# Optimization experiments

Hardware: AMD Instinct MI355X
Metric: run time of the kernel (lower is better)

The kernel has to match this reference:

```python
import jax, jax.numpy as jnp
import numpy as np

B, R, C, NH = 8, 64, 256, 8
N = R * R            # 4096 tokens
HD = C // NH         # head dim 32
FF = 3               # focusing factor

def dwconv(x, w, b):
    # x: (B, C, H, W); w: (C, 1, kh, kw) depthwise
    y = jax.lax.conv_general_dilated(
        x, w, window_strides=(1, 1), padding='SAME',
        dimension_numbers=('NCHW', 'OIHW', 'NCHW'),
        feature_group_count=x.shape[1])
    return y + b[None, :, None, None]

def setup_inputs() -> dict:
    key = jax.random.key(0)
    ks = jax.random.split(key, 6)
    return {
        'qkv': jax.random.normal(ks[0], (3, B, N, C), jnp.float32),
        'pos_enc': jax.random.normal(ks[1], (1, N, C), jnp.float32) * 0.02,
        'scale': jax.random.normal(ks[2], (1, 1, C), jnp.float32) * 0.02,
        'w_v': jax.random.normal(ks[3], (C, 1, 3, 3), jnp.float32) * 0.1,
        'b_v': jnp.zeros((C,), jnp.float32),
        'w_dwc': jax.random.normal(ks[4], (HD, 1, 5, 5), jnp.float32) * 0.1,
        'b_dwc': jnp.zeros((HD,), jnp.float32),
    }

def reference(qkv, pos_enc, scale, w_v, b_v, w_dwc, b_dwc):
    q, k, v = qkv[0], qkv[1], qkv[2]          # each (B, N, C)
    # --- LePE: depthwise 3x3 conv on v over full channel dim ---
    v_img = v.transpose(0, 2, 1).reshape(B, C, R, R)
    lepe = dwconv(v_img, w_v, b_v)            # (B, C, R, R)
    lepe = lepe.reshape(B * NH, HD, N).transpose(0, 2, 1)   # (B*h, N, hd)
    v = v_img.reshape(B, C, N).transpose(0, 2, 1)           # (B, N, C)
    # --- focused kernelization ---
    k = k + pos_enc
    sc = jax.nn.softplus(scale)
    q = (jax.nn.relu(q) + 1e-6) / sc
    k = (jax.nn.relu(k) + 1e-6) / sc
    qn = jnp.linalg.norm(q, axis=-1, keepdims=True)
    kn = jnp.linalg.norm(k, axis=-1, keepdims=True)
    q = q ** FF
    k = k ** FF
    q = q / jnp.linalg.norm(q, axis=-1, keepdims=True) * qn
    k = k / jnp.linalg.norm(k, axis=-1, keepdims=True) * kn
    split = lambda x: x.reshape(B, N, NH, HD).transpose(0, 2, 1, 3).reshape(B * NH, N, HD)
    q, k, v = split(q), split(k), split(v)    # (B*h, N, hd)
    # --- linear attention (kv aggregation path: N >> hd) ---
    z = 1.0 / (jnp.einsum('bic,bc->bi', q, k.sum(axis=1)) + 1e-6)
    kv = jnp.einsum('bjc,bjd->bcd', k, v)     # (B*h, hd, hd)
    x = jnp.einsum('bic,bcd,bi->bid', q, kv, z)
    # --- dwc feature mixing on v per head ---
    fm = v.transpose(0, 2, 1).reshape(B * NH, HD, R, R)
    fm = dwconv(fm, w_dwc, b_dwc).reshape(B * NH, HD, N).transpose(0, 2, 1)
    x = x + fm + lepe
    x = x.reshape(B, NH, N, HD).transpose(0, 2, 1, 3).reshape(B, N, C)
    return x
```

## Files before the change

### kernel.cpp

```cpp
#include <hip/hip_runtime.h>
#include <math.h>

#define B_  8
#define R_  64
#define C_  256
#define NH_ 8
#define N_  4096
#define HD_ 32
#define LDP 260

__device__ __forceinline__ float softplus_rcp(float s) {
    return 1.f / __logf(1.f + __expf(s));
}

__global__ __launch_bounds__(256) void kernelNB3(
        const float* __restrict__ qkv, const float* __restrict__ pos,
        const float* __restrict__ scale,
        float* __restrict__ qs_arr, float* __restrict__ part,
        float* __restrict__ kspart) {
    __shared__ float smem[8576];
    float* kf_s  = smem;
    float* v_s   = smem + 4160;
    float* rsc_s = smem + 8320;

    const int t    = threadIdx.x;
    const int wave = t >> 6, lane = t & 63;
    const int tk   = lane >> 4;
    const int lr   = lane & 15;
    const int blk  = blockIdx.x;
    const int tok0 = blk * 32;

    rsc_s[t] = softplus_rcp(scale[t]);

    const size_t qbase = (size_t)tok0 * C_;
    const size_t koff  = (size_t)B_ * N_ * C_;
    const size_t voff  = (size_t)2 * B_ * N_ * C_;

    const int h  = t >> 5;
    const int l  = t & 31;
    const int cg = l & 7;
    const int dg = l >> 3;

    float acc[4][8];
    #pragma unroll
    for (int ii = 0; ii < 4; ii++)
        #pragma unroll
        for (int jj = 0; jj < 8; jj++) acc[ii][jj] = 0.f;
    float ksp[4] = {0.f, 0.f, 0.f, 0.f};

    __syncthreads();
    float rs[16];
    #pragma unroll
    for (int j = 0; j < 4; j++)
        *(float4*)&rs[j * 4] = *(const float4*)&rsc_s[j * 64 + lr * 4];

    #pragma unroll
    for (int tile = 0; tile < 2; tile++) {
        const int row  = wave * 4 + tk;
        const int nrow = tile * 16 + row;
        const int tok  = tok0 + nrow;
        const size_t off  = qbase + (size_t)nrow * C_;
        const size_t poff = (size_t)(tok & (N_ - 1)) * C_;

        float kc[16];
        float sq2 = 0.f, sq6 = 0.f, sk2 = 0.f, sk6 = 0.f;
        #pragma unroll
        for (int j = 0; j < 4; j++) {
            const int c = j * 64 + lr * 4;
            const float4 q4 = *(const float4*)(qkv + off + c);
            const float4 k4 = *(const float4*)(qkv + koff + off + c);
            const float4 v4 = *(const float4*)(qkv + voff + off + c);
            const float4 p4 = *(const float4*)(pos + poff + c);
            *(float4*)&v_s[row * LDP + c] = v4;
            const float qa[4] = {q4.x, q4.y, q4.z, q4.w};
            const float ka[4] = {k4.x, k4.y, k4.z, k4.w};
            const float pa[4] = {p4.x, p4.y, p4.z, p4.w};
            #pragma unroll
            for (int e = 0; e < 4; e++) {
                const float r  = rs[j * 4 + e];
                const float qv = (fmaxf(qa[e], 0.f) + 1e-6f) * r;
                const float kw = (fmaxf(ka[e] + pa[e], 0.f) + 1e-6f) * r;
                sq2 += qv * qv;  sk2 += kw * kw;
                const float q3 = qv * qv * qv, k3 = kw * kw * kw;
                sq6 += q3 * q3;  sk6 += k3 * k3;
                kc[j * 4 + e] = k3;
            }
        }
        #pragma unroll
        for (int m = 1; m < 16; m <<= 1) {
            sq2 += __shfl_xor(sq2, m, 64);
            sq6 += __shfl_xor(sq6, m, 64);
            sk2 += __shfl_xor(sk2, m, 64);
            sk6 += __shfl_xor(sk6, m, 64);
        }
        if (lr == 0) qs_arr[tok] = sqrtf(sq2) * rsqrtf(sq6);
        const float ks = sqrtf(sk2) * rsqrtf(sk6);
        #pragma unroll
        for (int j = 0; j < 4; j++) {
            const float4 kf4 = make_float4(kc[j*4+0] * ks, kc[j*4+1] * ks,
                                           kc[j*4+2] * ks, kc[j*4+3] * ks);
            *(float4*)&kf_s[row * LDP + j * 64 + lr * 4] = kf4;
        }
        __syncthreads();
        {
            const float* kfp = kf_s + h * HD_ + cg * 4;
            const float* vp  = v_s  + h * HD_ + dg * 8;
            #pragma unroll 4
            for (int nl = 0; nl < 16; nl++) {
                const float4 kr = *(const float4*)(kfp + nl * LDP);
                const float4 va = *(const float4*)(vp  + nl * LDP);
                const float4 vb = *(const float4*)(vp  + nl * LDP + 4);
                ksp[0] += kr.x;  ksp[1] += kr.y;
                ksp[2] += kr.z;  ksp[3] += kr.w;
                const float kk[4] = {kr.x, kr.y, kr.z, kr.w};
                const float vv[8] = {va.x, va.y, va.z, va.w,
                                     vb.x, vb.y, vb.z, vb.w};
                #pragma unroll
                for (int ii = 0; ii < 4; ii++)
                    #pragma unroll
                    for (int jj = 0; jj < 8; jj++)
                        acc[ii][jj] = fmaf(kk[ii], vv[jj], acc[ii][jj]);
            }
        }
        __syncthreads();
    }

    #pragma unroll
    for (int ii = 0; ii < 4; ii++) {
        const float4 a = make_float4(acc[ii][0], acc[ii][1], acc[ii][2], acc[ii][3]);
        const float4 b = make_float4(acc[ii][4], acc[ii][5], acc[ii][6], acc[ii][7]);
        const int base = h * 1024 + (cg * 4 + ii) * 32 + dg * 8;
        *(float4*)&smem[base]     = a;
        *(float4*)&smem[base + 4] = b;
    }
    if (dg == 0)
        *(float4*)&kspart[(size_t)blk * 256 + h * 32 + cg * 4] =
            make_float4(ksp[0], ksp[1], ksp[2], ksp[3]);
    __syncthreads();
    float* pdst = part + (size_t)blk * 8192;
    #pragma unroll
    for (int i = 0; i < 8; i++)
        *(float4*)&pdst[i * 1024 + t * 4] = *(const float4*)&smem[i * 1024 + t * 4];
}

__global__ __launch_bounds__(256) void kernelR(
        const float* __restrict__ part, const float* __restrict__ kspart,
        float* __restrict__ kv_ws, float* __restrict__ ksum_ws) {
    const int t  = threadIdx.x;
    const int bh = blockIdx.x >> 2, q = blockIdx.x & 3;
    const int b  = bh >> 3, h = bh & 7;

    const float* p = part + (size_t)(b * 128) * 8192 + h * 1024 + q * 256 + t;
    float s = 0.f;
    #pragma unroll 4
    for (int j = 0; j < 128; j++) s += p[(size_t)j * 8192];
    kv_ws[bh * 1024 + q * 256 + t] = s;

    if (q == 0 && t < 32) {
        const float* kp = kspart + (size_t)(b * 128) * 256 + h * 32 + t;
        float s2 = 0.f;
        #pragma unroll 8
        for (int j = 0; j < 128; j++) s2 += kp[(size_t)j * 256];
        ksum_ws[bh * 32 + t] = s2;
    }
}

__global__ __launch_bounds__(256) void kernelCD2(
        const float* __restrict__ qkv, const float* __restrict__ qs_arr,
        const float* __restrict__ kv_ws, const float* __restrict__ ksum_ws,
        const float* __restrict__ scale,
        const float* __restrict__ w_v,  const float* __restrict__ b_v,
        const float* __restrict__ w_dwc, const float* __restrict__ b_dwc,
        float* __restrict__ out) {
    __shared__ float v_s[20 * 20 * 32];
    __shared__ float kv_s[1024];
    __shared__ float ks_s[32];
    __shared__ float rsc_s[32];
    const int t    = threadIdx.x;
    const int tile = blockIdx.x;
    const int h    = blockIdx.y;
    const int b    = blockIdx.z;
    const int ty0  = (tile >> 2) * 16, tx0 = (tile & 3) * 16;
    const int bh   = b * NH_ + h;

    ((float4*)kv_s)[t] = ((const float4*)(kv_ws + (size_t)bh * 1024))[t];
    if (t < 32) {
        ks_s[t]  = ksum_ws[bh * HD_ + t];
        rsc_s[t] = softplus_rcp(scale[h * HD_ + t]);
    }

    const float* vb = qkv + (size_t)2 * B_ * N_ * C_ + (size_t)b * N_ * C_ + h * HD_;
    #pragma unroll
    for (int i = 0; i < 13; i++) {
        const int idx = i * 256 + t;
        if (idx < 3200) {
            const int pix = idx >> 3, d4 = (idx & 7) * 4;
            const int yy = pix / 20, xx = pix - yy * 20;
            const int gy = ty0 + yy - 2, gx = tx0 + xx - 2;
            float4 val = make_float4(0.f, 0.f, 0.f, 0.f);
            if (gy >= 0 && gy < R_ && gx >= 0 && gx < R_)
                val = *(const float4*)(vb + (size_t)(gy * R_ + gx) * C_ + d4);
            *(float4*)&v_s[pix * 32 + d4] = val;
        }
    }

    const int c  = t & 31, pg = t >> 5;
    float wv[9], wd[25];
    {
        const float* wvp = w_v + (size_t)(h * HD_ + c) * 9;
        const float* wdp = w_dwc + (size_t)c * 25;
        #pragma unroll
        for (int i = 0; i < 9; i++)  wv[i] = wvp[i];
        #pragma unroll
        for (int i = 0; i < 25; i++) wd[i] = wdp[i];
    }
    const float bias = b_v[h * HD_ + c] + b_dwc[c];
    __syncthreads();

    float res[32];
    #pragma unroll
    for (int r2 = 0; r2 < 2; r2++) {
        const int ty = pg * 2 + r2;
        float win[5][5];
        #pragma unroll
        for (int j = 0; j < 5; j++)
            #pragma unroll
            for (int i = 0; i < 5; i++)
                win[j][i] = v_s[((ty + i) * 20 + j) * 32 + c];
        #pragma unroll
        for (int tx = 0; tx < 16; tx++) {
            float a = bias;
            #pragma unroll
            for (int j = 0; j < 5; j++) {
                const int slot = (tx + j) % 5;
                #pragma unroll
                for (int i = 0; i < 5; i++)
                    a = fmaf(wd[i * 5 + j], win[slot][i], a);
            }
            #pragma unroll
            for (int j = 1; j < 4; j++) {
                const int slot = (tx + j) % 5;
                #pragma unroll
                for (int i = 1; i < 4; i++)
                    a = fmaf(wv[(i - 1) * 3 + (j - 1)], win[slot][i], a);
            }
            res[r2 * 16 + tx] = a;
            if (tx < 15) {
                const int slot = tx % 5;
                #pragma unroll
                for (int i = 0; i < 5; i++)
                    win[slot][i] = v_s[((ty + i) * 20 + (tx + 5)) * 32 + c];
            }
        }
    }
    __syncthreads();
    #pragma unroll
    for (int r2 = 0; r2 < 2; r2++)
        #pragma unroll
        for (int tx = 0; tx < 16; tx++)
            v_s[((pg * 2 + r2) * 16 + tx) * 33 + c] = res[r2 * 16 + tx];
    __syncthreads();

    {
        const int tyy = t >> 4, txx = t & 15;
        const int n   = (ty0 + tyy) * R_ + (tx0 + txx);
        const int tok = b * N_ + n;
        float q[32];
        const float4* qsrc = (const float4*)(qkv + (size_t)tok * C_ + h * HD_);
        #pragma unroll
        for (int i = 0; i < 8; i++) ((float4*)q)[i] = qsrc[i];
        const float qs = qs_arr[tok];
        #pragma unroll
        for (int i = 0; i < 32; i++) {
            const float r = (fmaxf(q[i], 0.f) + 1e-6f) * rsc_s[i];
            q[i] = r * r * r * qs;
        }

        float denom = 1e-6f;
        #pragma unroll
        for (int cc = 0; cc < 32; cc++) denom = fmaf(q[cc], ks_s[cc], denom);
        const float z = 1.f / denom;

        float o[32];
        #pragma unroll
        for (int i = 0; i < 32; i++) o[i] = 0.f;
        #pragma unroll
        for (int cc = 0; cc < 32; cc++) {
            const float qc = q[cc];
            #pragma unroll
            for (int d = 0; d < 32; d++)
                o[d] = fmaf(qc, kv_s[cc * 32 + d], o[d]);
        }
        float4* dst = (float4*)(out + (size_t)tok * C_ + h * HD_);
        #pragma unroll
        for (int i = 0; i < 8; i++) {
            float4 v4;
            v4.x = fmaf(o[i*4+0], z, v_s[t * 33 + i*4+0]);
            v4.y = fmaf(o[i*4+1], z, v_s[t * 33 + i*4+1]);
            v4.z = fmaf(o[i*4+2], z, v_s[t * 33 + i*4+2]);
            v4.w = fmaf(o[i*4+3], z, v_s[t * 33 + i*4+3]);
            dst[i] = v4;
        }
    }
}

extern "C" void kernel_launch(void* const* d_in, const int* in_sizes, int n_in,
                              void* d_out, int out_size, void* d_ws, size_t ws_size,
                              hipStream_t stream) {
    const float* qkv   = (const float*)d_in[0];
    const float* pos   = (const float*)d_in[1];
    const float* scale = (const float*)d_in[2];
    const float* w_v   = (const float*)d_in[3];
    const float* b_v   = (const float*)d_in[4];
    const float* w_dwc = (const float*)d_in[5];
    const float* b_dwc = (const float*)d_in[6];
    float* out = (float*)d_out;

    float* qs_arr  = (float*)d_ws;
    float* part    = qs_arr + (size_t)B_ * N_;
    float* kspart  = part + (size_t)1024 * 8192;
    float* kv_ws   = kspart + (size_t)1024 * 256;
    float* ksum_ws = kv_ws + 64 * 1024;

    kernelNB3<<<dim3(1024), 256, 0, stream>>>(qkv, pos, scale, qs_arr, part, kspart);
    kernelR<<<dim3(256), 256, 0, stream>>>(part, kspart, kv_ws, ksum_ws);
    kernelCD2<<<dim3(16, NH_, B_), 256, 0, stream>>>(qkv, qs_arr, kv_ws, ksum_ws,
                                                     scale, w_v, b_v, w_dwc, b_dwc, out);
}
```

Before: 228.9 us.

## Double-buffer kv aggregation tiles and halve block count with 64 tokens each

```diff
diff --git a/kernel.cpp b/kernel.cpp
--- a/kernel.cpp
+++ b/kernel.cpp
@@ -13,22 +13,21 @@
     return 1.f / __logf(1.f + __expf(s));
 }
 
-__global__ __launch_bounds__(256) void kernelNB3(
+__global__ __launch_bounds__(256) void kernelNB4(
         const float* __restrict__ qkv, const float* __restrict__ pos,
         const float* __restrict__ scale,
         float* __restrict__ qs_arr, float* __restrict__ part,
         float* __restrict__ kspart) {
-    __shared__ float smem[8576];
-    float* kf_s  = smem;
-    float* v_s   = smem + 4160;
-    float* rsc_s = smem + 8320;
+    __shared__ float smem[16896];
+    float* rsc_s = smem + 16640;
 
     const int t    = threadIdx.x;
     const int wave = t >> 6, lane = t & 63;
     const int tk   = lane >> 4;
     const int lr   = lane & 15;
     const int blk  = blockIdx.x;
-    const int tok0 = blk * 32;
+    const int tok0 = blk * 64;
+    const int row  = wave * 4 + tk;
 
     rsc_s[t] = softplus_rcp(scale[t]);
 
@@ -48,36 +47,38 @@
         for (int jj = 0; jj < 8; jj++) acc[ii][jj] = 0.f;
     float ksp[4] = {0.f, 0.f, 0.f, 0.f};
 
-    __syncthreads();
-    float rs[16];
-    #pragma unroll
-    for (int j = 0; j < 4; j++)
-        *(float4*)&rs[j * 4] = *(const float4*)&rsc_s[j * 64 + lr * 4];
-
-    #pragma unroll
-    for (int tile = 0; tile < 2; tile++) {
-        const int row  = wave * 4 + tk;
-        const int nrow = tile * 16 + row;
-        const int tok  = tok0 + nrow;
+    float4 sq[4], sk[4], sv[4], sp[4];
+
+    auto LOAD = [&](int tt) {
+        const int    nrow = tt * 16 + row;
         const size_t off  = qbase + (size_t)nrow * C_;
-        const size_t poff = (size_t)(tok & (N_ - 1)) * C_;
-
+        const size_t poff = (size_t)((tok0 + nrow) & (N_ - 1)) * C_;
+        #pragma unroll
+        for (int j = 0; j < 4; j++) {
+            const int c = j * 64 + lr * 4;
+            sq[j] = *(const float4*)(qkv + off + c);
+            sk[j] = *(const float4*)(qkv + koff + off + c);
+            sv[j] = *(const float4*)(qkv + voff + off + c);
+            sp[j] = *(const float4*)(pos + poff + c);
+        }
+    };
+
+    auto PROC = [&](int tt) {
+        float* kf_s = (tt & 1) ? smem + 4160  : smem;
+        float* v_s  = (tt & 1) ? smem + 12480 : smem + 8320;
+        const int tok = tok0 + tt * 16 + row;
         float kc[16];
         float sq2 = 0.f, sq6 = 0.f, sk2 = 0.f, sk6 = 0.f;
         #pragma unroll
         for (int j = 0; j < 4; j++) {
             const int c = j * 64 + lr * 4;
-            const float4 q4 = *(const float4*)(qkv + off + c);
-            const float4 k4 = *(const float4*)(qkv + koff + off + c);
-            const float4 v4 = *(const float4*)(qkv + voff + off + c);
-            const float4 p4 = *(const float4*)(pos + poff + c);
-            *(float4*)&v_s[row * LDP + c] = v4;
-            const float qa[4] = {q4.x, q4.y, q4.z, q4.w};
-            const float ka[4] = {k4.x, k4.y, k4.z, k4.w};
-            const float pa[4] = {p4.x, p4.y, p4.z, p4.w};
+            *(float4*)&v_s[row * LDP + c] = sv[j];
+            const float qa[4] = {sq[j].x, sq[j].y, sq[j].z, sq[j].w};
+            const float ka[4] = {sk[j].x, sk[j].y, sk[j].z, sk[j].w};
+            const float pa[4] = {sp[j].x, sp[j].y, sp[j].z, sp[j].w};
             #pragma unroll
             for (int e = 0; e < 4; e++) {
-                const float r  = rs[j * 4 + e];
+                const float r  = rsc_s[c + e];
                 const float qv = (fmaxf(qa[e], 0.f) + 1e-6f) * r;
                 const float kw = (fmaxf(ka[e] + pa[e], 0.f) + 1e-6f) * r;
                 sq2 += qv * qv;  sk2 += kw * kw;
@@ -101,29 +102,44 @@
                                            kc[j*4+2] * ks, kc[j*4+3] * ks);
             *(float4*)&kf_s[row * LDP + j * 64 + lr * 4] = kf4;
         }
-        __syncthreads();
-        {
-            const float* kfp = kf_s + h * HD_ + cg * 4;
-            const float* vp  = v_s  + h * HD_ + dg * 8;
-            #pragma unroll 4
-            for (int nl = 0; nl < 16; nl++) {
-                const float4 kr = *(const float4*)(kfp + nl * LDP);
-                const float4 va = *(const float4*)(vp  + nl * LDP);
-                const float4 vb = *(const float4*)(vp  + nl * LDP + 4);
-                ksp[0] += kr.x;  ksp[1] += kr.y;
-                ksp[2] += kr.z;  ksp[3] += kr.w;
-                const float kk[4] = {kr.x, kr.y, kr.z, kr.w};
-                const float vv[8] = {va.x, va.y, va.z, va.w,
-                                     vb.x, vb.y, vb.z, vb.w};
+    };
+
+    auto COMP = [&](int tt) {
+        const float* kf_s = (tt & 1) ? smem + 4160  : smem;
+        const float* v_s  = (tt & 1) ? smem + 12480 : smem + 8320;
+        const float* kfp = kf_s + h * HD_ + cg * 4;
+        const float* vp  = v_s  + h * HD_ + dg * 8;
+        #pragma unroll 4
+        for (int nl = 0; nl < 16; nl++) {
+            const float4 kr = *(const float4*)(kfp + nl * LDP);
+            const float4 va = *(const float4*)(vp  + nl * LDP);
+            const float4 vb = *(const float4*)(vp  + nl * LDP + 4);
+            ksp[0] += kr.x;  ksp[1] += kr.y;
+            ksp[2] += kr.z;  ksp[3] += kr.w;
+            const float kk[4] = {kr.x, kr.y, kr.z, kr.w};
+            const float vv[8] = {va.x, va.y, va.z, va.w,
+                                 vb.x, vb.y, vb.z, vb.w};
+            #pragma unroll
+            for (int ii = 0; ii < 4; ii++)
                 #pragma unroll
-                for (int ii = 0; ii < 4; ii++)
-                    #pragma unroll
-                    for (int jj = 0; jj < 8; jj++)
-                        acc[ii][jj] = fmaf(kk[ii], vv[jj], acc[ii][jj]);
-            }
-        }
-        __syncthreads();
-    }
+                for (int jj = 0; jj < 8; jj++)
+                    acc[ii][jj] = fmaf(kk[ii], vv[jj], acc[ii][jj]);
+        }
+    };
+
+    LOAD(0);
+    __syncthreads();
+    PROC(0);
+    LOAD(1);
+    __syncthreads();
+    #pragma unroll
+    for (int tt = 0; tt < 4; tt++) {
+        COMP(tt);
+        if (tt < 3) PROC(tt + 1);
+        if (tt < 2) LOAD(tt + 2);
+        if (tt < 3) __syncthreads();
+    }
+    __syncthreads();
 
     #pragma unroll
     for (int ii = 0; ii < 4; ii++) {
@@ -150,17 +166,17 @@
     const int bh = blockIdx.x >> 2, q = blockIdx.x & 3;
     const int b  = bh >> 3, h = bh & 7;
 
-    const float* p = part + (size_t)(b * 128) * 8192 + h * 1024 + q * 256 + t;
+    const float* p = part + (size_t)(b * 64) * 8192 + h * 1024 + q * 256 + t;
     float s = 0.f;
     #pragma unroll 4
-    for (int j = 0; j < 128; j++) s += p[(size_t)j * 8192];
+    for (int j = 0; j < 64; j++) s += p[(size_t)j * 8192];
     kv_ws[bh * 1024 + q * 256 + t] = s;
 
     if (q == 0 && t < 32) {
-        const float* kp = kspart + (size_t)(b * 128) * 256 + h * 32 + t;
+        const float* kp = kspart + (size_t)(b * 64) * 256 + h * 32 + t;
         float s2 = 0.f;
         #pragma unroll 8
-        for (int j = 0; j < 128; j++) s2 += kp[(size_t)j * 256];
+        for (int j = 0; j < 64; j++) s2 += kp[(size_t)j * 256];
         ksum_ws[bh * 32 + t] = s2;
     }
 }
@@ -318,11 +334,11 @@
 
     float* qs_arr  = (float*)d_ws;
     float* part    = qs_arr + (size_t)B_ * N_;
-    float* kspart  = part + (size_t)1024 * 8192;
-    float* kv_ws   = kspart + (size_t)1024 * 256;
+    float* kspart  = part + (size_t)512 * 8192;
+    float* kv_ws   = kspart + (size_t)512 * 256;
     float* ksum_ws = kv_ws + 64 * 1024;
 
-    kernelNB3<<<dim3(1024), 256, 0, stream>>>(qkv, pos, scale, qs_arr, part, kspart);
+    kernelNB4<<<dim3(512), 256, 0, stream>>>(qkv, pos, scale, qs_arr, part, kspart);
     kernelR<<<dim3(256), 256, 0, stream>>>(part, kspart, kv_ws, ksum_ws);
     kernelCD2<<<dim3(16, NH_, B_), 256, 0, stream>>>(qkv, qs_arr, kv_ws, ksum_ws,
                                                      scale, w_v, b_v, w_dwc, b_dwc, out);
```

After: 223.1 us. -2.5%, faster.
